# Performance work log

Measured on AMD Instinct MI355X. Metric: run time of the kernel, lower is better.

## Reference

```python
import jax, jax.numpy as jnp
import numpy as np
from jax import lax

NEG = -1e9
B, H, C, TX, TY = 4, 256, 80, 256, 1024  # batch, hidden, mel bins, text len, mel len


def setup_inputs() -> dict:
    key = jax.random.key(0)
    k = jax.random.split(key, 6)
    en = jax.random.normal(k[0], (B, H, TX), jnp.float32)
    mu = jax.random.normal(k[1], (B, C, TX), jnp.float32)
    log_sigma = 0.1 * jax.random.normal(k[2], (B, C, TX), jnp.float32)
    y = jax.random.normal(k[3], (B, C, TY), jnp.float32)
    x_lengths = jax.random.randint(k[4], (B,), TX // 2, TX + 1, jnp.int32)
    y_lengths = jax.random.randint(k[5], (B,), TY // 2, TY + 1, jnp.int32)
    return {"en": en, "mu": mu, "log_sigma": log_sigma, "y": y,
            "x_lengths": x_lengths, "y_lengths": y_lengths}


def sequence_mask(lengths, max_len):
    return jnp.arange(max_len)[None, :] < lengths[:, None]


def compute_log_probs(mu, log_sigma, y):
    # y: [B,C,Ty] -> [B,1,Ty,C]; mu/log_sigma: [B,C,Tx] -> [B,Tx,1,C]
    yb = jnp.transpose(y, (0, 2, 1))[:, None]
    mub = jnp.transpose(mu, (0, 2, 1))[:, :, None]
    lsb = jnp.transpose(log_sigma, (0, 2, 1))[:, :, None]
    # mse / sigma^2 = (y-mu)^2 * exp(-2*log_sigma); mean over channel dim
    expo = -0.5 * jnp.mean((yb - mub) ** 2 * jnp.exp(-2.0 * lsb), axis=-1)  # [B,Tx,Ty]
    return expo - 0.5 * jnp.mean(lsb, axis=-1)  # broadcast [B,Tx,1] -> [B,Tx,Ty]


def maximum_path(logp, mask, x_lengths, y_lengths):
    """Monotonic alignment search (Glow-TTS Viterbi DP), vectorized over batch."""
    b, tx, ty = logp.shape
    lp = jnp.where(mask > 0, logp, NEG)
    cols = jnp.moveaxis(lp, 2, 0)  # [Ty, B, Tx]
    v0 = jnp.broadcast_to(jnp.where(jnp.arange(tx) == 0, 0.0, NEG), (b, tx)).astype(logp.dtype)

    def fwd(v, col):
        v_shift = jnp.concatenate([jnp.full((b, 1), NEG, v.dtype), v[:, :-1]], axis=1)
        diag = v_shift > v  # come from (x-1, y-1) rather than (x, y-1)
        return col + jnp.maximum(v, v_shift), diag

    _, diags = lax.scan(fwd, v0, cols)  # diags: [Ty, B, Tx] bool

    xs_idx = jnp.arange(tx)

    def bwd(idx, inp):
        yv, dcol = inp
        active = yv < y_lengths  # [B]
        row = (xs_idx[None, :] == idx[:, None]) & active[:, None]
        d = jnp.take_along_axis(dcol, idx[:, None], axis=1)[:, 0]
        idx = jnp.where(active & (idx > 0) & d, idx - 1, idx)
        return idx, row

    _, rows = lax.scan(bwd, x_lengths - 1, (jnp.arange(ty), diags), reverse=True)
    return lax.stop_gradient(jnp.moveaxis(rows, 0, 2).astype(logp.dtype))  # [B,Tx,Ty]


def generate_path(dr, mask):
    # dr: [B,Tx] durations; mask: [B,Tx,Ty]
    ty = mask.shape[-1]
    cum = jnp.cumsum(dr, axis=1)
    pm = (jnp.arange(ty)[None, None, :] < cum[:, :, None]).astype(dr.dtype)
    path = pm - jnp.pad(pm, ((0, 0), (1, 0), (0, 0)))[:, :-1]
    return path * mask


def reference(en, mu, log_sigma, y, x_lengths, y_lengths):
    tx, ty = mu.shape[-1], y.shape[-1]
    x_mask = sequence_mask(x_lengths, tx).astype(jnp.float32)  # [B,Tx]
    y_mask = sequence_mask(y_lengths, ty).astype(jnp.float32)  # [B,Ty]
    attn_mask = x_mask[:, :, None] * y_mask[:, None, :]        # [B,Tx,Ty]
    logp = compute_log_probs(mu, log_sigma, y)
    attn = maximum_path(logp, attn_mask, x_lengths, y_lengths)
    dr_mas = jnp.sum(attn, axis=-1)                            # durations [B,Tx]
    path = generate_path(dr_mas, attn_mask)                    # convert_dr_to_align
    # expand_encoder_outputs: attn^T @ en^T -> [B,H,Ty]
    o_en_ex = jnp.einsum('bxy,bhx->bhy', path, en)
    return o_en_ex, logp, attn, dr_mas
```

## Files before the change

### kernel.cpp

```cpp
#include <hip/hip_runtime.h>
#include <cstdint>
#include <cmath>

#define B_ 4
#define H_ 256
#define C_ 80
#define TX_ 256
#define TY_ 1024
#define NC_ 64
#define NEGF (-1e9f)

#define OFF_LOGP (B_*H_*TY_)
#define OFF_ATTN (OFF_LOGP + B_*TX_*TY_)
#define OFF_DR   (OFF_ATTN + B_*TX_*TY_)

__device__ __forceinline__ float dpp_shr1_negfill_f32(float x) {
  union { float f; int i; } u, o, r;
  u.f = x; o.f = NEGF;
  r.i = __builtin_amdgcn_update_dpp(o.i, u.i, 0x138, 0xf, 0xf, false);
  return r.f;
}

__global__ __launch_bounds__(256) void k_logp(
    const float* __restrict__ mu, const float* __restrict__ ls,
    const float* __restrict__ y, const int* __restrict__ xlp,
    const int* __restrict__ ylp, float* __restrict__ logp_out,
    float* __restrict__ lpT)
{
  const int b  = blockIdx.y;
  const int x0 = blockIdx.x * 4;
  const int tid = threadIdx.x;
  __shared__ double s_w[4][C_];
  __shared__ double s_m1[4][C_];
  __shared__ double s_wm2[4][C_];
  __shared__ double s_lsv[4][C_];
  __shared__ double s_K[4];
  __shared__ double s_t0[4];
  __shared__ float tile[TY_][4];
  for (int i = tid; i < 4 * C_; i += 256) {
    int xi = i / C_, c = i - xi * C_;
    double m = (double)mu[(b * C_ + c) * TX_ + x0 + xi];
    double l = (double)ls[(b * C_ + c) * TX_ + x0 + xi];
    double w = exp(-2.0 * l);
    s_w[xi][c]   = w;
    s_m1[xi][c]  = -2.0 * w * m;
    s_wm2[xi][c] = w * m * m;
    s_lsv[xi][c] = l;
  }
  __syncthreads();
  {
    int xi = tid >> 6, cc = tid & 63;
    double kp = (cc < C_) ? s_wm2[xi][cc] : 0.0;
    double tp = (cc < C_) ? s_lsv[xi][cc] : 0.0;
    if (cc + 64 < C_) { kp += s_wm2[xi][cc + 64]; tp += s_lsv[xi][cc + 64]; }
#pragma unroll
    for (int off = 32; off; off >>= 1) {
      kp += __shfl_down(kp, off);
      tp += __shfl_down(tp, off);
    }
    if (cc == 0) { s_K[xi] = kp; s_t0[xi] = -0.5 * (tp * (1.0 / C_)); }
  }
  __syncthreads();

  const int t0 = tid * 4;
  double acc[4][4];
#pragma unroll
  for (int xi = 0; xi < 4; ++xi)
#pragma unroll
    for (int k = 0; k < 4; ++k) acc[xi][k] = 0.0;

  const float4* yp = (const float4*)(y + (size_t)b * C_ * TY_) + tid;
#pragma unroll 4
  for (int c = 0; c < C_; ++c) {
    float4 yv = yp[c * (TY_ / 4)];
    double y0 = yv.x, y1 = yv.y, y2 = yv.z, y3 = yv.w;
#pragma unroll
    for (int xi = 0; xi < 4; ++xi) {
      double w = s_w[xi][c], m1 = s_m1[xi][c];
      double u0 = fma(w, y0, m1), u1 = fma(w, y1, m1);
      double u2 = fma(w, y2, m1), u3 = fma(w, y3, m1);
      acc[xi][0] = fma(u0, y0, acc[xi][0]);
      acc[xi][1] = fma(u1, y1, acc[xi][1]);
      acc[xi][2] = fma(u2, y2, acc[xi][2]);
      acc[xi][3] = fma(u3, y3, acc[xi][3]);
    }
  }

  const int xlen = xlp[b], ylen = ylp[b];
#pragma unroll
  for (int xi = 0; xi < 4; ++xi) {
    int x = x0 + xi;
    double c0 = s_t0[xi], K = s_K[xi];
    float r[4];
#pragma unroll
    for (int k = 0; k < 4; ++k)
      r[k] = (float)((acc[xi][k] + K) * (-0.5 / C_) + c0);
    *(float4*)&logp_out[((size_t)(b * TX_ + x)) * TY_ + t0] =
        make_float4(r[0], r[1], r[2], r[3]);
    bool xm = x < xlen;
#pragma unroll
    for (int k = 0; k < 4; ++k)
      tile[t0 + k][xi] = (xm && (t0 + k) < ylen) ? r[k] : NEGF;
  }
  __syncthreads();

  float* dst = lpT + (size_t)b * TY_ * TX_ + x0;
  const float4* tp = (const float4*)tile;
#pragma unroll
  for (int k = 0; k < 4; ++k) {
    int t = tid + 256 * k;
    *(float4*)&dst[(size_t)t * TX_] = tp[t];
  }
}

#define PHASE_BAR() \
  asm volatile("s_waitcnt lgkmcnt(0)\n\ts_barrier" ::: "memory")

#define PHASEQ(FL, FC, q)                                                   \
  {                                                                         \
    const int cl = (q) - w;                                                 \
    const int clc = cl < 0 ? 0 : (cl >= NC_ ? NC_ - 1 : cl);                \
    const float* cb = gb + (size_t)clc * 16 * TX_ + tid;                    \
    _Pragma("unroll")                                                       \
    for (int i = 0; i < 16; ++i) FL[i] = cb[i * TX_];    \
    const int cc = (q) - 3 - w;                                             \
    if (cc >= 0 && cc < NC_) {                                              \
      if (cc == 0) { v = (tid == 0) ? 0.0f : NEGF; word = 0u; }             \
      const uint32_t bitbase = 1u << ((cc & 1) << 4);                       \
      float* wr = (lane == 63) ? &bdry[cc & 1][w + 1][0] : &dummy[lane];    \
      const float* bp = &bdry[cc & 1][w][0];                                \
      float bv[16];                                                         \
      *(float4*)&bv[0]  = *(const float4*)(bp);                             \
      *(float4*)&bv[4]  = *(const float4*)(bp + 4);                         \
      *(float4*)&bv[8]  = *(const float4*)(bp + 8);                         \
      *(float4*)&bv[12] = *(const float4*)(bp + 12);                        \
      wr[0] = v;                                                            \
      _Pragma("unroll")                                                     \
      for (int i = 0; i < 16; ++i) {                                        \
        float vl = dpp_shr1_negfill_f32(v);                                 \
        if (amlane0) vl = bv[i];                                            \
        if (vl > v) word |= (bitbase << i);                                 \
        float nv = FC[i] + fmaxf(v, vl);                                    \
        if (i < 15) wr[i + 1] = nv;                                         \
        v = nv;                                                             \
      }                                                                     \
      if (cc & 1) { bits[(cc >> 1) * 256 + tid] = word; word = 0u; }        \
    }                                                                       \
    PHASE_BAR();                                                            \
  }

__global__ __launch_bounds__(256, 1) void k_dp(
    const float* __restrict__ lpT, const int* __restrict__ xlp,
    const int* __restrict__ ylp, float* __restrict__ dr_out,
    int* __restrict__ cum_ws, int* __restrict__ xt_ws)
{
  const int b = blockIdx.x;
  const int tid = threadIdx.x;
  const int lane = tid & 63;
  const int w = tid >> 6;
  __shared__ uint32_t bits[8192];
  __shared__ uint32_t dur[TX_];
  __shared__ float bdry[2][5][16];
  __shared__ float dummy[80];

  const float* gb = lpT + (size_t)b * TY_ * TX_;
  const bool amlane0 = (w > 0) && (lane == 0);

  float v = NEGF;
  uint32_t word = 0;
  float f0[16], f1[16], f2[16], f3[16];

  for (int q = 0; q < 72; q += 4) {
    PHASEQ(f0, f1, q);
    PHASEQ(f1, f2, q + 1);
    PHASEQ(f2, f3, q + 2);
    PHASEQ(f3, f0, q + 3);
  }
  __syncthreads();

  dur[tid] = 0;
  __syncthreads();

  const int xlen = xlp[b], ylen = ylp[b];
  if (tid == 0) {
    int idx = xlen - 1;
    int t = ylen - 1;
    while (t >= 0) {
      if (idx == 0) { dur[0] = (uint32_t)(t + 1); break; }
      int ww = t >> 5, rr = t & 31;
      uint32_t wd = bits[ww * 256 + idx];
      wd &= (rr == 31) ? 0xffffffffu : ((1u << (rr + 1)) - 1u);
      while (wd == 0 && ww > 0) { --ww; wd = bits[ww * 256 + idx]; }
      if (wd == 0) { dur[idx] = (uint32_t)(t + 1); break; }
      int bitpos = 31 - __builtin_clz(wd);
      int tp = (ww << 5) | bitpos;
      dur[idx] = (uint32_t)(t - tp + 1);
      --idx;
      t = tp - 1;
    }
  }
  __syncthreads();

  if (w == 0) {
    uint32_t d0 = dur[4 * lane], d1 = dur[4 * lane + 1];
    uint32_t d2 = dur[4 * lane + 2], d3 = dur[4 * lane + 3];
    uint32_t own = d0 + d1 + d2 + d3;
    uint32_t s = own;
#pragma unroll
    for (int off = 1; off < 64; off <<= 1) {
      uint32_t n = __shfl_up(s, off);
      if (lane >= off) s += n;
    }
    uint32_t base = s - own;
    uint32_t c0 = base + d0, c1 = c0 + d1, c2 = c1 + d2, c3 = c2 + d3;
    int x = 4 * lane;
    cum_ws[b * TX_ + x]     = (int)c0;
    cum_ws[b * TX_ + x + 1] = (int)c1;
    cum_ws[b * TX_ + x + 2] = (int)c2;
    cum_ws[b * TX_ + x + 3] = (int)c3;
    dr_out[b * TX_ + x]     = (float)d0;
    dr_out[b * TX_ + x + 1] = (float)d1;
    dr_out[b * TX_ + x + 2] = (float)d2;
    dr_out[b * TX_ + x + 3] = (float)d3;
    int* xt = xt_ws + b * TY_;
    for (uint32_t t = c0 - d0; t < c0; ++t) xt[t] = x;
    for (uint32_t t = c1 - d1; t < c1; ++t) xt[t] = x + 1;
    for (uint32_t t = c2 - d2; t < c2; ++t) xt[t] = x + 2;
    for (uint32_t t = c3 - d3; t < c3; ++t) xt[t] = x + 3;
  }
}

__global__ __launch_bounds__(256) void k_epi(
    const int* __restrict__ cum_ws, const int* __restrict__ xt_ws,
    const float* __restrict__ en, const int* __restrict__ ylp,
    float* __restrict__ attn, float* __restrict__ oen)
{
  const int b = blockIdx.y, bx = blockIdx.x, tid = threadIdx.x;
  __shared__ float row[TX_];
  if (bx < TX_) {
    const int x = bx;
    int hi = cum_ws[b * TX_ + x];
    int lo = (x > 0) ? cum_ws[b * TX_ + x - 1] : 0;
    int t0 = tid * 4;
    float4 v;
    v.x = (t0     >= lo && t0     < hi) ? 1.f : 0.f;
    v.y = (t0 + 1 >= lo && t0 + 1 < hi) ? 1.f : 0.f;
    v.z = (t0 + 2 >= lo && t0 + 2 < hi) ? 1.f : 0.f;
    v.w = (t0 + 3 >= lo && t0 + 3 < hi) ? 1.f : 0.f;
    *(float4*)&attn[((size_t)(b * TX_ + x)) * TY_ + t0] = v;
  } else {
    const int h = bx - TX_;
    row[tid] = en[((size_t)(b * H_ + h)) * TX_ + tid];
    __syncthreads();
    const int ylen = ylp[b];
    int t0 = tid * 4;
    int4 xi = *(const int4*)&xt_ws[b * TY_ + t0];
    float4 v;
    v.x = (t0     < ylen) ? row[xi.x & (TX_ - 1)] : 0.f;
    v.y = (t0 + 1 < ylen) ? row[xi.y & (TX_ - 1)] : 0.f;
    v.z = (t0 + 2 < ylen) ? row[xi.z & (TX_ - 1)] : 0.f;
    v.w = (t0 + 3 < ylen) ? row[xi.w & (TX_ - 1)] : 0.f;
    *(float4*)&oen[((size_t)(b * H_ + h)) * TY_ + t0] = v;
  }
}

extern "C" void kernel_launch(void* const* d_in, const int* in_sizes, int n_in,
                              void* d_out, int out_size, void* d_ws, size_t ws_size,
                              hipStream_t stream)
{
  const float* en = (const float*)d_in[0];
  const float* mu = (const float*)d_in[1];
  const float* ls = (const float*)d_in[2];
  const float* y  = (const float*)d_in[3];
  const int*   xl = (const int*)d_in[4];
  const int*   yl = (const int*)d_in[5];

  float* out  = (float*)d_out;
  float* oen  = out;
  float* logp = out + OFF_LOGP;
  float* attn = out + OFF_ATTN;
  float* dr   = out + OFF_DR;

  int* cum = (int*)d_ws;
  int* xt  = cum + B_ * TX_;

  k_logp<<<dim3(TX_ / 4, B_),   256, 0, stream>>>(mu, ls, y, xl, yl, logp, attn);
  k_dp  <<<B_,                  256, 0, stream>>>(attn, xl, yl, dr, cum, xt);
  k_epi <<<dim3(TX_ + H_, B_),  256, 0, stream>>>(cum, xt, en, yl, attn, oen);
}
```

Baseline: 184.3 us.

## Drop transposed masked logp copy; DP reads logp rows directly with in-kernel masking

The logp kernel no longer writes a masked, transposed copy of logp into the attn buffer through a shared-memory tile. Instead, each DP thread reads its own contiguous logp row as float4 vectors and applies the x/y length mask in registers. The boundary writes from lane 63 are batched into float4 stores, replacing the per-step dummy-pointer stores. This removes a full B*Tx*Ty write and the LDS transpose, at the cost of strided, per-thread row reads in the latency-bound 4-block DP kernel.

New measurement: 192.1 us. 4.3% more time.

```diff
diff --git a/kernel.cpp b/kernel.cpp
--- a/kernel.cpp
+++ b/kernel.cpp
@@ -23,9 +23,7 @@
 
 __global__ __launch_bounds__(256) void k_logp(
     const float* __restrict__ mu, const float* __restrict__ ls,
-    const float* __restrict__ y, const int* __restrict__ xlp,
-    const int* __restrict__ ylp, float* __restrict__ logp_out,
-    float* __restrict__ lpT)
+    const float* __restrict__ y, float* __restrict__ logp_out)
 {
   const int b  = blockIdx.y;
   const int x0 = blockIdx.x * 4;
@@ -36,7 +34,6 @@
   __shared__ double s_lsv[4][C_];
   __shared__ double s_K[4];
   __shared__ double s_t0[4];
-  __shared__ float tile[TY_][4];
   for (int i = tid; i < 4 * C_; i += 256) {
     int xi = i / C_, c = i - xi * C_;
     double m = (double)mu[(b * C_ + c) * TX_ + x0 + xi];
@@ -86,7 +83,6 @@
     }
   }
 
-  const int xlen = xlp[b], ylen = ylp[b];
 #pragma unroll
   for (int xi = 0; xi < 4; ++xi) {
     int x = x0 + xi;
@@ -97,19 +93,6 @@
       r[k] = (float)((acc[xi][k] + K) * (-0.5 / C_) + c0);
     *(float4*)&logp_out[((size_t)(b * TX_ + x)) * TY_ + t0] =
         make_float4(r[0], r[1], r[2], r[3]);
-    bool xm = x < xlen;
-#pragma unroll
-    for (int k = 0; k < 4; ++k)
-      tile[t0 + k][xi] = (xm && (t0 + k) < ylen) ? r[k] : NEGF;
-  }
-  __syncthreads();
-
-  float* dst = lpT + (size_t)b * TY_ * TX_ + x0;
-  const float4* tp = (const float4*)tile;
-#pragma unroll
-  for (int k = 0; k < 4; ++k) {
-    int t = tid + 256 * k;
-    *(float4*)&dst[(size_t)t * TX_] = tp[t];
   }
 }
 
@@ -120,29 +103,42 @@
   {                                                                         \
     const int cl = (q) - w;                                                 \
     const int clc = cl < 0 ? 0 : (cl >= NC_ ? NC_ - 1 : cl);                \
-    const float* cb = gb + (size_t)clc * 16 * TX_ + tid;                    \
-    _Pragma("unroll")                                                       \
-    for (int i = 0; i < 16; ++i) FL[i] = cb[i * TX_];    \
+    const float4* cb = (const float4*)(myrow + clc * 16);                   \
+    FL[0] = cb[0]; FL[1] = cb[1]; FL[2] = cb[2]; FL[3] = cb[3];             \
     const int cc = (q) - 3 - w;                                             \
     if (cc >= 0 && cc < NC_) {                                              \
       if (cc == 0) { v = (tid == 0) ? 0.0f : NEGF; word = 0u; }             \
       const uint32_t bitbase = 1u << ((cc & 1) << 4);                       \
-      float* wr = (lane == 63) ? &bdry[cc & 1][w + 1][0] : &dummy[lane];    \
       const float* bp = &bdry[cc & 1][w][0];                                \
       float bv[16];                                                         \
       *(float4*)&bv[0]  = *(const float4*)(bp);                             \
       *(float4*)&bv[4]  = *(const float4*)(bp + 4);                         \
       *(float4*)&bv[8]  = *(const float4*)(bp + 8);                         \
       *(float4*)&bv[12] = *(const float4*)(bp + 12);                        \
-      wr[0] = v;                                                            \
+      const int tb = cc * 16;                                               \
+      float fv[16];                                                         \
+      _Pragma("unroll")                                                     \
+      for (int i = 0; i < 16; ++i) {                                        \
+        float raw = ((const float*)FC)[i];                                  \
+        fv[i] = (xm && (tb + i) < ylen) ? raw : NEGF;                       \
+      }                                                                     \
+      float bs[16];                                                         \
+      bs[0] = v;                                                            \
       _Pragma("unroll")                                                     \
       for (int i = 0; i < 16; ++i) {                                        \
         float vl = dpp_shr1_negfill_f32(v);                                 \
         if (amlane0) vl = bv[i];                                            \
         if (vl > v) word |= (bitbase << i);                                 \
-        float nv = FC[i] + fmaxf(v, vl);                                    \
-        if (i < 15) wr[i + 1] = nv;                                         \
+        float nv = fv[i] + fmaxf(v, vl);                                    \
+        if (i < 15) bs[i + 1] = nv;                                         \
         v = nv;                                                             \
+      }                                                                     \
+      if (lane == 63) {                                                     \
+        float* wr = &bdry[cc & 1][w + 1][0];                                \
+        *(float4*)(wr)      = *(float4*)&bs[0];                             \
+        *(float4*)(wr + 4)  = *(float4*)&bs[4];                             \
+        *(float4*)(wr + 8)  = *(float4*)&bs[8];                             \
+        *(float4*)(wr + 12) = *(float4*)&bs[12];                            \
       }                                                                     \
       if (cc & 1) { bits[(cc >> 1) * 256 + tid] = word; word = 0u; }        \
     }                                                                       \
@@ -150,9 +146,10 @@
   }
 
 __global__ __launch_bounds__(256, 1) void k_dp(
-    const float* __restrict__ lpT, const int* __restrict__ xlp,
-    const int* __restrict__ ylp, float* __restrict__ dr_out,
-    int* __restrict__ cum_ws, int* __restrict__ xt_ws)
+    const float* lpg,
+    const int* __restrict__ xlp, const int* __restrict__ ylp,
+    float* __restrict__ dr_out, int* __restrict__ cum_ws,
+    int* __restrict__ xt_ws)
 {
   const int b = blockIdx.x;
   const int tid = threadIdx.x;
@@ -161,14 +158,15 @@
   __shared__ uint32_t bits[8192];
   __shared__ uint32_t dur[TX_];
   __shared__ float bdry[2][5][16];
-  __shared__ float dummy[80];
-
-  const float* gb = lpT + (size_t)b * TY_ * TX_;
+
+  const float* myrow = lpg + ((size_t)(b * TX_ + tid)) * TY_;
+  const int xlen = xlp[b], ylen = ylp[b];
+  const bool xm = tid < xlen;
   const bool amlane0 = (w > 0) && (lane == 0);
 
   float v = NEGF;
   uint32_t word = 0;
-  float f0[16], f1[16], f2[16], f3[16];
+  float4 f0[4], f1[4], f2[4], f3[4];
 
   for (int q = 0; q < 72; q += 4) {
     PHASEQ(f0, f1, q);
@@ -181,7 +179,6 @@
   dur[tid] = 0;
   __syncthreads();
 
-  const int xlen = xlp[b], ylen = ylp[b];
   if (tid == 0) {
     int idx = xlen - 1;
     int t = ylen - 1;
@@ -284,7 +281,7 @@
   int* cum = (int*)d_ws;
   int* xt  = cum + B_ * TX_;
 
-  k_logp<<<dim3(TX_ / 4, B_),   256, 0, stream>>>(mu, ls, y, xl, yl, logp, attn);
-  k_dp  <<<B_,                  256, 0, stream>>>(attn, xl, yl, dr, cum, xt);
+  k_logp<<<dim3(TX_ / 4, B_),   256, 0, stream>>>(mu, ls, y, logp);
+  k_dp  <<<B_,                  256, 0, stream>>>(logp, xl, yl, dr, cum, xt);
   k_epi <<<dim3(TX_ + H_, B_),  256, 0, stream>>>(cum, xt, en, yl, attn, oen);
 }
```
